# Kernel optimization log

Hardware: AMD Instinct MI355X
Metric: run time of the kernel (lower is better)

The kernel has to match this reference:

```python
import jax, jax.numpy as jnp
import numpy as np

B, O, K, GS = 4096, 11008, 4096, 128  # batch, out_features, in_features, group_size
G = K // GS  # num groups = 32


def _unpack_int4(packed):
    """packed: [N, K//2] int values in [0,256) holding two 4-bit nibbles (low first).
    Returns signed int4 values as float32 [N, K]."""
    low = packed & 15
    high = (packed >> 4) & 15
    q = jnp.stack([low, high], axis=-1).reshape(packed.shape[0], -1)  # interleave low,high
    return jnp.where(q >= 8, q - 16, q).astype(jnp.float32)


def setup_inputs() -> dict:
    key = jax.random.key(0)
    k1, k2, k3, k4, k5 = jax.random.split(key, 5)
    x = jax.random.randint(k1, (B, K // 2), 0, 256, dtype=jnp.int32)
    a_scale = jax.random.uniform(k2, (B, G), dtype=jnp.float32).astype(jnp.float16)
    w_packed = jax.random.randint(k3, (O, K // 2), 0, 256, dtype=jnp.int32)
    w_scale = jax.random.uniform(k4, (O, G), dtype=jnp.float32).astype(jnp.float16)
    bias = (jax.random.normal(k5, (O,), dtype=jnp.float32) * 0.02).astype(jnp.float16)
    return {"x": x, "a_scale": a_scale, "w_packed": w_packed, "w_scale": w_scale,
            "bias": bias, "group_size": GS}


def reference(x, a_scale, w_packed, w_scale, bias, group_size):
    # out[b,o] = sum_g a_scale[b,g] * w_scale[o,g] * sum_{k in g} x_int4[b,k] * w_int4[o,k] + bias[o]
    # Fold the per-group scales into the dequantized operands, then a single GEMM
    # (mathematically identical to group-wise int accumulate + dequant).
    b, o = x.shape[0], w_packed.shape[0]
    k = x.shape[1] * 2
    g = k // group_size
    xq = _unpack_int4(x).reshape(b, g, group_size) * a_scale.astype(jnp.float32)[:, :, None]
    wq = _unpack_int4(w_packed).reshape(o, g, group_size) * w_scale.astype(jnp.float32)[:, :, None]
    out = jnp.einsum('bgk,ogk->bo', xq, wq).astype(jnp.float16)  # [B, O] fp16
    return out + bias
```

## Files before the change

### kernel.cpp

```cpp
#include <hip/hip_runtime.h>


#define B_DIM 4096
#define O_DIM 11008
#define K_DIM 4096
#define G_NUM 32

#define NX32 8388608u
#define NW32 22544384u
#define X8_BYTES  16777216u
#define W8_BYTES  45088768u

typedef int   i32x4 __attribute__((ext_vector_type(4)));
typedef float f32x4 __attribute__((ext_vector_type(4)));

__device__ __forceinline__ unsigned pack2(int v) {
    int t = v ^ 0x88;
    unsigned lo = (unsigned)(((t & 15) - 8) & 0xFF);
    unsigned hi = (unsigned)((((t >> 4) & 15) - 8) & 0xFF);
    return lo | (hi << 8);
}

__global__ __launch_bounds__(256)
void unpack_kernel(const int* __restrict__ xq, const int* __restrict__ wq,
                   unsigned char* __restrict__ X8, unsigned char* __restrict__ W8) {
    unsigned t = blockIdx.x * 256u + threadIdx.x;
    const int* src;
    unsigned char* dst;
    if (t < NX32 / 8) {
        src = xq + (size_t)t * 8;
        dst = X8 + (size_t)t * 16;
    } else {
        unsigned j = t - NX32 / 8;
        src = wq + (size_t)j * 8;
        dst = W8 + (size_t)j * 16;
    }
    int4 v0 = ((const int4*)src)[0];
    int4 v1 = ((const int4*)src)[1];
    uint4 o;
    o.x = pack2(v0.x) | (pack2(v0.y) << 16);
    o.y = pack2(v0.z) | (pack2(v0.w) << 16);
    o.z = pack2(v1.x) | (pack2(v1.y) << 16);
    o.w = pack2(v1.z) | (pack2(v1.w) << 16);
    *(uint4*)dst = o;
}

__global__ __launch_bounds__(256)
void tscale_kernel(const float* __restrict__ as_, const float* __restrict__ ws_,
                   float* __restrict__ asT, float* __restrict__ wsT) {
    __shared__ float tile[64][33];
    const int blk = blockIdx.x, t = threadIdx.x;
    const float* src; float* dst; int R0, RTOT;
    if (blk < 64) { src = as_; dst = asT; R0 = blk * 64;        RTOT = B_DIM; }
    else          { src = ws_; dst = wsT; R0 = (blk - 64) * 64; RTOT = O_DIM; }
    {
        const int r = t >> 2, cc = (t & 3) * 8;
        const float* p = src + (size_t)(R0 + r) * G_NUM + cc;
        f32x4 v0 = *(const f32x4*)p;
        f32x4 v1 = *(const f32x4*)(p + 4);
#pragma unroll
        for (int k = 0; k < 4; ++k) { tile[r][cc + k] = v0[k]; tile[r][cc + 4 + k] = v1[k]; }
    }
    __syncthreads();
    {
        const int g = t >> 3, bc = (t & 7) * 8;
        f32x4 w0, w1;
#pragma unroll
        for (int k = 0; k < 4; ++k) { w0[k] = tile[bc + k][g]; w1[k] = tile[bc + 4 + k][g]; }
        float* q = dst + (size_t)g * RTOT + R0 + bc;
        *(f32x4*)q = w0;
        *(f32x4*)(q + 4) = w1;
    }
}

__global__ __launch_bounds__(256, 2)
void gemm_i8(const unsigned char* __restrict__ X8, const unsigned char* __restrict__ W8,
             const float* __restrict__ asT, const float* __restrict__ wsT,
             const float* __restrict__ bias, float* __restrict__ out) {
    __shared__ __align__(16) unsigned char A0[16384];
    __shared__ __align__(16) unsigned char B0[16384];
    __shared__ __align__(16) unsigned char A1[16384];
    __shared__ __align__(16) unsigned char B1[16384];

    const int tid  = threadIdx.x;
    const int wv   = tid >> 6;
    const int lane = tid & 63;
    const int quad = lane >> 4;
    const int lq   = lane & 15;
    const int bm   = blockIdx.x;
    const int bn   = blockIdx.y;
    const int wm   = (wv & 1) << 6;
    const int wn   = (wv >> 1) << 6;

    f32x4 facc[4][4] = {};

    const int l8 = lane >> 3;
    const int c8 = lane & 7;
    const int sw_chunk = ((c8 ^ l8) << 4);
    const size_t xrow0 = (size_t)(bm * 128) * K_DIM;
    const size_t wrow0 = (size_t)(bn * 128) * K_DIM;
    const int abase = bm * 128 + wm + (quad << 2);
    const int wbase = bn * 128 + wn + lq;
    const int pa0 = ((quad ^ (lq & 7)) << 4);
    const int pa1 = (((4 + quad) ^ (lq & 7)) << 4);

    auto stageAB = [&](int g, unsigned char* Ad, unsigned char* Bd) {
        const int gb = g << 7;
#pragma unroll
        for (int s = 0; s < 4; ++s) {
            const int slab = (wv << 2) + s;
            const int row  = (slab << 3) + l8;
            const unsigned char* gpA = X8 + xrow0 + (size_t)row * K_DIM + gb + sw_chunk;
            __builtin_amdgcn_global_load_lds(
                (const __attribute__((address_space(1))) void*)gpA,
                (__attribute__((address_space(3))) void*)(Ad + (slab << 10)), 16, 0, 0);
        }
#pragma unroll
        for (int s = 0; s < 4; ++s) {
            const int slab = (wv << 2) + s;
            const int row  = (slab << 3) + l8;
            const unsigned char* gpB = W8 + wrow0 + (size_t)row * K_DIM + gb + sw_chunk;
            __builtin_amdgcn_global_load_lds(
                (const __attribute__((address_space(1))) void*)gpB,
                (__attribute__((address_space(3))) void*)(Bd + (slab << 10)), 16, 0, 0);
        }
    };
    auto loadScales = [&](int g, f32x4 (&asr)[4], float (&wsn)[4]) {
#pragma unroll
        for (int i = 0; i < 4; ++i)
            asr[i] = *(const f32x4*)&asT[(g << 12) + abase + (i << 4)];
#pragma unroll
        for (int j = 0; j < 4; ++j)
            wsn[j] = wsT[(size_t)g * O_DIM + wbase + (j << 4)];
    };

    f32x4 asrA[4], asrB[4];
    float wsnA[4], wsnB[4];

    auto body = [&](int g, const unsigned char* Ac, const unsigned char* Bc,
                    unsigned char* An, unsigned char* Bn,
                    f32x4 (&asrC)[4], float (&wsnC)[4],
                    f32x4 (&asrN)[4], float (&wsnN)[4]) {
        const int gn = (g + 1 < G_NUM) ? g + 1 : G_NUM - 1;
        i32x4 gacc[4][4] = {};
        i32x4 av0[4], bv0[4], av1[4], bv1[4];

        asm volatile("s_waitcnt vmcnt(8)" ::: "memory");
        __builtin_amdgcn_s_barrier();
        __builtin_amdgcn_sched_barrier(0);

#pragma unroll
        for (int i = 0; i < 4; ++i)
            av0[i] = *(const i32x4*)&Ac[((wm + (i << 4) + lq) << 7) + pa0];
#pragma unroll
        for (int j = 0; j < 4; ++j)
            bv0[j] = *(const i32x4*)&Bc[((wn + (j << 4) + lq) << 7) + pa0];
        stageAB(gn, An, Bn);

        asm volatile("s_waitcnt lgkmcnt(0)" ::: "memory");
        __builtin_amdgcn_sched_barrier(0);
        __builtin_amdgcn_s_setprio(1);
#pragma unroll
        for (int i = 0; i < 4; ++i)
#pragma unroll
            for (int j = 0; j < 4; ++j)
                gacc[i][j] = __builtin_amdgcn_mfma_i32_16x16x64_i8(av0[i], bv0[j], gacc[i][j], 0, 0, 0);
        __builtin_amdgcn_s_setprio(0);

#pragma unroll
        for (int i = 0; i < 4; ++i)
            av1[i] = *(const i32x4*)&Ac[((wm + (i << 4) + lq) << 7) + pa1];
#pragma unroll
        for (int j = 0; j < 4; ++j)
            bv1[j] = *(const i32x4*)&Bc[((wn + (j << 4) + lq) << 7) + pa1];
        asm volatile("s_waitcnt lgkmcnt(0)" ::: "memory");
        __builtin_amdgcn_sched_barrier(0);
        __builtin_amdgcn_s_setprio(1);
#pragma unroll
        for (int i = 0; i < 4; ++i)
#pragma unroll
            for (int j = 0; j < 4; ++j)
                gacc[i][j] = __builtin_amdgcn_mfma_i32_16x16x64_i8(av1[i], bv1[j], gacc[i][j], 0, 0, 0);
        __builtin_amdgcn_s_setprio(0);

        asm volatile("s_waitcnt vmcnt(8)" ::: "memory");
        __builtin_amdgcn_sched_barrier(0);
#pragma unroll
        for (int i = 0; i < 4; ++i)
#pragma unroll
            for (int j = 0; j < 4; ++j) {
                f32x4 s = asrC[i] * wsnC[j];
                f32x4 gf;
#pragma unroll
                for (int r = 0; r < 4; ++r) gf[r] = (float)gacc[i][j][r];
                facc[i][j] += gf * s;
            }
        loadScales(gn, asrN, wsnN);
    };

    stageAB(0, A0, B0);
    loadScales(0, asrA, wsnA);

#pragma unroll 1
    for (int g2 = 0; g2 < G_NUM; g2 += 2) {
        body(g2,     A0, B0, A1, B1, asrA, wsnA, asrB, wsnB);
        body(g2 + 1, A1, B1, A0, B0, asrB, wsnB, asrA, wsnA);
    }

    const int n0 = bn * 128 + wn + lq;
    const int m0 = bm * 128 + wm + (quad << 2);
    float bvs[4];
#pragma unroll
    for (int j = 0; j < 4; ++j) bvs[j] = bias[n0 + (j << 4)];
#pragma unroll
    for (int i = 0; i < 4; ++i) {
#pragma unroll
        for (int r = 0; r < 4; ++r) {
            float* orow = out + (size_t)(m0 + (i << 4) + r) * O_DIM;
#pragma unroll
            for (int j = 0; j < 4; ++j)
                orow[n0 + (j << 4)] = facc[i][j][r] + bvs[j];
        }
    }
}

extern "C" void kernel_launch(void* const* d_in, const int* in_sizes, int n_in,
                              void* d_out, int out_size, void* d_ws, size_t ws_size,
                              hipStream_t stream) {
    const int*   xq   = (const int*)d_in[0];
    const float* as_  = (const float*)d_in[1];
    const int*   wq   = (const int*)d_in[2];
    const float* ws_  = (const float*)d_in[3];
    const float* bias = (const float*)d_in[4];
    float* out        = (float*)d_out;

    unsigned char* X8 = (unsigned char*)d_ws;
    unsigned char* W8 = X8 + X8_BYTES;
    float* asT = (float*)((unsigned char*)d_ws + X8_BYTES + W8_BYTES);
    float* wsT = asT + (size_t)G_NUM * B_DIM;

    unpack_kernel<<<(NX32 + NW32) / 8 / 256, 256, 0, stream>>>(xq, wq, X8, W8);
    tscale_kernel<<<64 + 172, 256, 0, stream>>>(as_, ws_, asT, wsT);
    gemm_i8<<<dim3(B_DIM / 128, O_DIM / 128), 256, 0, stream>>>(X8, W8, asT, wsT, bias, out);
}
```

Measured before the change: 544.9 us.

## Enlarge int8 GEMM block tile to 256x256 with 8 waves and LDS-staged scales

The GEMM block tile grows from 128x128 with 4 waves to 256x256 with 8 waves, and each wave now covers a 128x64 sub-tile. The goal is to double operand reuse per byte loaded from global memory. Per-group scales are now loaded asynchronously into LDS alongside the operand tiles instead of into registers. The inner loop is also reorganised to run the MFMAs one A-row at a time, prefetching the next row's fragments. In exchange, LDS grows to about 132KB, which allows only one block per CU. The pipeline now relies on __syncthreads instead of partial vmcnt waits, which may serialise loads and compute more.

```diff
diff --git a/kernel.cpp b/kernel.cpp
--- a/kernel.cpp
+++ b/kernel.cpp
@@ -13,6 +13,10 @@
 
 typedef int   i32x4 __attribute__((ext_vector_type(4)));
 typedef float f32x4 __attribute__((ext_vector_type(4)));
+
+#define GLOAD16(src, dst) __builtin_amdgcn_global_load_lds(                      \
+    (const __attribute__((address_space(1))) void*)(src),                        \
+    (__attribute__((address_space(3))) void*)(dst), 16, 0, 0)
 
 __device__ __forceinline__ unsigned pack2(int v) {
     int t = v ^ 0x88;
@@ -73,14 +77,18 @@
     }
 }
 
-__global__ __launch_bounds__(256, 2)
+__global__ __launch_bounds__(512, 2)
 void gemm_i8(const unsigned char* __restrict__ X8, const unsigned char* __restrict__ W8,
              const float* __restrict__ asT, const float* __restrict__ wsT,
              const float* __restrict__ bias, float* __restrict__ out) {
-    __shared__ __align__(16) unsigned char A0[16384];
-    __shared__ __align__(16) unsigned char B0[16384];
-    __shared__ __align__(16) unsigned char A1[16384];
-    __shared__ __align__(16) unsigned char B1[16384];
+    __shared__ __align__(16) unsigned char A0[32768];
+    __shared__ __align__(16) unsigned char B0[32768];
+    __shared__ __align__(16) unsigned char A1[32768];
+    __shared__ __align__(16) unsigned char B1[32768];
+    __shared__ __align__(16) float SA0[256];
+    __shared__ __align__(16) float SW0[256];
+    __shared__ __align__(16) float SA1[256];
+    __shared__ __align__(16) float SW1[256];
 
     const int tid  = threadIdx.x;
     const int wv   = tid >> 6;
@@ -89,131 +97,110 @@
     const int lq   = lane & 15;
     const int bm   = blockIdx.x;
     const int bn   = blockIdx.y;
-    const int wm   = (wv & 1) << 6;
+    const int wm   = (wv & 1) << 7;
     const int wn   = (wv >> 1) << 6;
 
-    f32x4 facc[4][4] = {};
-
-    const int l8 = lane >> 3;
-    const int c8 = lane & 7;
-    const int sw_chunk = ((c8 ^ l8) << 4);
-    const size_t xrow0 = (size_t)(bm * 128) * K_DIM;
-    const size_t wrow0 = (size_t)(bn * 128) * K_DIM;
-    const int abase = bm * 128 + wm + (quad << 2);
-    const int wbase = bn * 128 + wn + lq;
+    f32x4 facc[8][4] = {};
+
+    const size_t xrow0 = (size_t)(bm * 256) * K_DIM;
+    const size_t wrow0 = (size_t)(bn * 256) * K_DIM;
     const int pa0 = ((quad ^ (lq & 7)) << 4);
     const int pa1 = (((4 + quad) ^ (lq & 7)) << 4);
 
+    const int r8 = tid >> 3;
+    const int c8 = tid & 7;
+    const int sw = ((c8 ^ (r8 & 7)) << 4);
+    const int ldsw = (wv << 10);
+
     auto stageAB = [&](int g, unsigned char* Ad, unsigned char* Bd) {
         const int gb = g << 7;
 #pragma unroll
-        for (int s = 0; s < 4; ++s) {
-            const int slab = (wv << 2) + s;
-            const int row  = (slab << 3) + l8;
-            const unsigned char* gpA = X8 + xrow0 + (size_t)row * K_DIM + gb + sw_chunk;
-            __builtin_amdgcn_global_load_lds(
-                (const __attribute__((address_space(1))) void*)gpA,
-                (__attribute__((address_space(3))) void*)(Ad + (slab << 10)), 16, 0, 0);
-        }
-#pragma unroll
-        for (int s = 0; s < 4; ++s) {
-            const int slab = (wv << 2) + s;
-            const int row  = (slab << 3) + l8;
-            const unsigned char* gpB = W8 + wrow0 + (size_t)row * K_DIM + gb + sw_chunk;
-            __builtin_amdgcn_global_load_lds(
-                (const __attribute__((address_space(1))) void*)gpB,
-                (__attribute__((address_space(3))) void*)(Bd + (slab << 10)), 16, 0, 0);
+        for (int p = 0; p < 4; ++p) {
+            const int row = (p << 6) + r8;
+            GLOAD16(X8 + xrow0 + (size_t)row * K_DIM + gb + sw, Ad + (p << 13) + ldsw);
+        }
+#pragma unroll
+        for (int p = 0; p < 4; ++p) {
+            const int row = (p << 6) + r8;
+            GLOAD16(W8 + wrow0 + (size_t)row * K_DIM + gb + sw, Bd + (p << 13) + ldsw);
         }
     };
-    auto loadScales = [&](int g, f32x4 (&asr)[4], float (&wsn)[4]) {
-#pragma unroll
-        for (int i = 0; i < 4; ++i)
-            asr[i] = *(const f32x4*)&asT[(g << 12) + abase + (i << 4)];
-#pragma unroll
-        for (int j = 0; j < 4; ++j)
-            wsn[j] = wsT[(size_t)g * O_DIM + wbase + (j << 4)];
+    auto stageScales = [&](int g, float* sAn, float* sWn) {
+        if (wv == 0) {
+            GLOAD16(asT + (size_t)g * B_DIM + bm * 256 + (lane << 2), sAn);
+        } else if (wv == 1) {
+            GLOAD16(wsT + (size_t)g * O_DIM + bn * 256 + (lane << 2), sWn);
+        }
     };
 
-    f32x4 asrA[4], asrB[4];
-    float wsnA[4], wsnB[4];
-
-    auto body = [&](int g, const unsigned char* Ac, const unsigned char* Bc,
-                    unsigned char* An, unsigned char* Bn,
-                    f32x4 (&asrC)[4], float (&wsnC)[4],
-                    f32x4 (&asrN)[4], float (&wsnN)[4]) {
-        const int gn = (g + 1 < G_NUM) ? g + 1 : G_NUM - 1;
-        i32x4 gacc[4][4] = {};
-        i32x4 av0[4], bv0[4], av1[4], bv1[4];
-
-        asm volatile("s_waitcnt vmcnt(8)" ::: "memory");
-        __builtin_amdgcn_s_barrier();
-        __builtin_amdgcn_sched_barrier(0);
-
-#pragma unroll
-        for (int i = 0; i < 4; ++i)
-            av0[i] = *(const i32x4*)&Ac[((wm + (i << 4) + lq) << 7) + pa0];
-#pragma unroll
-        for (int j = 0; j < 4; ++j)
+    auto body = [&](int gnext,
+                    const unsigned char* Ac, const unsigned char* Bc,
+                    const float* sAc, const float* sWc,
+                    unsigned char* An, unsigned char* Bn, float* sAn, float* sWn) {
+        __syncthreads();
+        stageAB(gnext, An, Bn);
+        stageScales(gnext, sAn, sWn);
+
+        i32x4 bv0[4], bv1[4];
+        float wsn[4];
+#pragma unroll
+        for (int j = 0; j < 4; ++j) {
             bv0[j] = *(const i32x4*)&Bc[((wn + (j << 4) + lq) << 7) + pa0];
-        stageAB(gn, An, Bn);
-
-        asm volatile("s_waitcnt lgkmcnt(0)" ::: "memory");
-        __builtin_amdgcn_sched_barrier(0);
-        __builtin_amdgcn_s_setprio(1);
-#pragma unroll
-        for (int i = 0; i < 4; ++i)
+            bv1[j] = *(const i32x4*)&Bc[((wn + (j << 4) + lq) << 7) + pa1];
+            wsn[j] = sWc[wn + (j << 4) + lq];
+        }
+        i32x4 a0c = *(const i32x4*)&Ac[((wm + lq) << 7) + pa0];
+        i32x4 a1c = *(const i32x4*)&Ac[((wm + lq) << 7) + pa1];
+        f32x4 sac = *(const f32x4*)&sAc[wm + (quad << 2)];
+
+#pragma unroll
+        for (int i = 0; i < 8; ++i) {
+            asm volatile("s_waitcnt lgkmcnt(0)" ::: "memory");
+            __builtin_amdgcn_sched_barrier(0);
+            const i32x4 a0 = a0c, a1 = a1c;
+            const f32x4 sa = sac;
+            if (i < 7) {
+                a0c = *(const i32x4*)&Ac[((wm + ((i + 1) << 4) + lq) << 7) + pa0];
+                a1c = *(const i32x4*)&Ac[((wm + ((i + 1) << 4) + lq) << 7) + pa1];
+                sac = *(const f32x4*)&sAc[wm + ((i + 1) << 4) + (quad << 2)];
+            }
+            i32x4 q[4];
+            __builtin_amdgcn_s_setprio(1);
 #pragma unroll
             for (int j = 0; j < 4; ++j)
-                gacc[i][j] = __builtin_amdgcn_mfma_i32_16x16x64_i8(av0[i], bv0[j], gacc[i][j], 0, 0, 0);
-        __builtin_amdgcn_s_setprio(0);
-
-#pragma unroll
-        for (int i = 0; i < 4; ++i)
-            av1[i] = *(const i32x4*)&Ac[((wm + (i << 4) + lq) << 7) + pa1];
-#pragma unroll
-        for (int j = 0; j < 4; ++j)
-            bv1[j] = *(const i32x4*)&Bc[((wn + (j << 4) + lq) << 7) + pa1];
-        asm volatile("s_waitcnt lgkmcnt(0)" ::: "memory");
-        __builtin_amdgcn_sched_barrier(0);
-        __builtin_amdgcn_s_setprio(1);
-#pragma unroll
-        for (int i = 0; i < 4; ++i)
+                q[j] = __builtin_amdgcn_mfma_i32_16x16x64_i8(a0, bv0[j], (i32x4){0, 0, 0, 0}, 0, 0, 0);
 #pragma unroll
             for (int j = 0; j < 4; ++j)
-                gacc[i][j] = __builtin_amdgcn_mfma_i32_16x16x64_i8(av1[i], bv1[j], gacc[i][j], 0, 0, 0);
-        __builtin_amdgcn_s_setprio(0);
-
-        asm volatile("s_waitcnt vmcnt(8)" ::: "memory");
-        __builtin_amdgcn_sched_barrier(0);
-#pragma unroll
-        for (int i = 0; i < 4; ++i)
+                q[j] = __builtin_amdgcn_mfma_i32_16x16x64_i8(a1, bv1[j], q[j], 0, 0, 0);
+            __builtin_amdgcn_s_setprio(0);
 #pragma unroll
             for (int j = 0; j < 4; ++j) {
-                f32x4 s = asrC[i] * wsnC[j];
+                const f32x4 s = sa * wsn[j];
                 f32x4 gf;
 #pragma unroll
-                for (int r = 0; r < 4; ++r) gf[r] = (float)gacc[i][j][r];
+                for (int r = 0; r < 4; ++r) gf[r] = (float)q[j][r];
                 facc[i][j] += gf * s;
             }
-        loadScales(gn, asrN, wsnN);
+        }
     };
 
     stageAB(0, A0, B0);
-    loadScales(0, asrA, wsnA);
+    stageScales(0, SA0, SW0);
 
 #pragma unroll 1
     for (int g2 = 0; g2 < G_NUM; g2 += 2) {
-        body(g2,     A0, B0, A1, B1, asrA, wsnA, asrB, wsnB);
-        body(g2 + 1, A1, B1, A0, B0, asrB, wsnB, asrA, wsnA);
-    }
-
-    const int n0 = bn * 128 + wn + lq;
-    const int m0 = bm * 128 + wm + (quad << 2);
+        const int gn2 = (g2 + 2 < G_NUM) ? g2 + 2 : G_NUM - 1;
+        body(g2 + 1, A0, B0, SA0, SW0, A1, B1, SA1, SW1);
+        body(gn2,    A1, B1, SA1, SW1, A0, B0, SA0, SW0);
+    }
+
+    const int n0 = bn * 256 + wn + lq;
+    const int m0 = bm * 256 + wm + (quad << 2);
     float bvs[4];
 #pragma unroll
     for (int j = 0; j < 4; ++j) bvs[j] = bias[n0 + (j << 4)];
 #pragma unroll
-    for (int i = 0; i < 4; ++i) {
+    for (int i = 0; i < 8; ++i) {
 #pragma unroll
         for (int r = 0; r < 4; ++r) {
             float* orow = out + (size_t)(m0 + (i << 4) + r) * O_DIM;
@@ -241,5 +228,5 @@
 
     unpack_kernel<<<(NX32 + NW32) / 8 / 256, 256, 0, stream>>>(xq, wq, X8, W8);
     tscale_kernel<<<64 + 172, 256, 0, stream>>>(as_, ws_, asT, wsT);
-    gemm_i8<<<dim3(B_DIM / 128, O_DIM / 128), 256, 0, stream>>>(X8, W8, asT, wsT, bias, out);
-}
+    gemm_i8<<<dim3(B_DIM / 256, O_DIM / 256), 512, 0, stream>>>(X8, W8, asT, wsT, bias, out);
+}
```

New measurement: 1.567 ms. 188% more time.
